# Optimization experiments

Hardware: AMD Instinct MI355X
Metric: run time of the kernel (lower is better)

The kernel has to match this reference:

```python
import math
import jax, jax.numpy as jnp
import numpy as np

B, T, D, S = 4, 8192, 1024, 32  # batch, seq, dim, num_slots; segment L = T // S


def setup_inputs() -> dict:
    key = jax.random.key(0)
    ks = jax.random.split(key, 11)
    d_inv_sqrt = D ** -0.5
    return {
        "x": jax.random.normal(ks[0], (B, T, D), jnp.float32),
        "gate_w": jax.random.normal(ks[1], (D, D), jnp.float32) * d_inv_sqrt,
        "gate_b": jnp.zeros((D,), jnp.float32),
        "read_q_w": jax.random.normal(ks[2], (D, D), jnp.float32) * 0.02,
        "read_k_w": jax.random.normal(ks[3], (D, D), jnp.float32) * 0.02,
        "read_v_w": jax.random.normal(ks[4], (D, D), jnp.float32) * 0.02,
        "output_w": jax.random.normal(ks[5], (D, D), jnp.float32) * d_inv_sqrt,
        "memory_slots": jax.random.normal(ks[6], (S, D), jnp.float32) * 0.02,
        "write_q_w": jax.random.normal(ks[7], (D, D), jnp.float32) * 0.02,
        "write_k_w": jax.random.normal(ks[8], (D, D), jnp.float32) * 0.02,
        "write_v_w": jax.random.normal(ks[9], (D, D), jnp.float32) * 0.02,
    }


def reference(x, gate_w, gate_b, read_q_w, read_k_w, read_v_w, output_w,
              memory_slots, write_q_w, write_k_w, write_v_w):
    b, t, d = x.shape
    s = memory_slots.shape[0]
    L = t // s  # segment length
    scale = 1.0 / math.sqrt(d)

    h = x @ gate_w.T + gate_b  # [B,T,D] gate pre-activation

    # --- write: per-slot attention over that slot's segment (block-diagonal) ---
    q = memory_slots @ write_q_w.T                      # [S,D]
    xs = x.reshape(b, s, L, d)                          # [B,S,L,D]
    k = xs @ write_k_w.T                                # [B,S,L,D]
    v = xs @ write_v_w.T                                # [B,S,L,D]
    wqk = jnp.einsum('sd,bsld->bsl', q, k) * scale      # [B,S,L]
    wattn = jax.nn.softmax(wqk, axis=-1)
    memory = jnp.einsum('bsl,bsld->bsd', wattn, v)      # [B,S,D]

    # --- read: masked cross-attention from tokens to memory slots ---
    rq = x @ read_q_w.T                                 # [B,T,D]
    rk = memory @ read_k_w.T                            # [B,S,D]
    rv = memory @ read_v_w.T                            # [B,S,D]
    rqk = jnp.einsum('btd,bsd->bts', rq, rk) * scale    # [B,T,S]
    seg = jnp.arange(t) // L                            # token -> segment index
    mask = seg[:, None] <= jnp.arange(s)[None, :]       # [T,S]; attend to slots >= own segment
    rqk = jnp.where(mask[None, :, :], rqk, -jnp.inf)
    rattn = jax.nn.softmax(rqk, axis=-1)
    read = jnp.einsum('bts,bsd->btd', rattn, rv)        # [B,T,D]

    y = x + jax.nn.sigmoid(h) * read
    out = y @ output_w.T
    return out, memory
```

## Files before the change

### kernel.cpp

```cpp
#include <hip/hip_runtime.h>
#include <stdint.h>

#define TB 4
#define TT 8192
#define TD 1024
#define TS 32
#define TL 256
#define BT 32768

typedef unsigned short u16;
typedef __bf16 bf16x8 __attribute__((ext_vector_type(8)));
typedef float f32x4 __attribute__((ext_vector_type(4)));

typedef uint32_t u32_g __attribute__((address_space(1)));
typedef uint32_t u32_l __attribute__((address_space(3)));

#define VMWAIT(N) asm volatile("s_waitcnt vmcnt(" #N ")" ::: "memory")
#define LGKM0()   asm volatile("s_waitcnt lgkmcnt(0)" ::: "memory")

__device__ __forceinline__ u16 f2b(float f){
  union { float f; uint32_t u; } a; a.f = f;
  uint32_t r = a.u + 0x7FFFu + ((a.u >> 16) & 1u);
  return (u16)(r >> 16);
}
__device__ __forceinline__ float b2f(u16 u){
  union { uint32_t u; float f; } a; a.u = ((uint32_t)u) << 16;
  return a.f;
}
__device__ __forceinline__ void gll16(const void* g, void* l){
  __builtin_amdgcn_global_load_lds((const u32_g*)g, (u32_l*)l, 16, 0, 0);
}

__global__ void k_convw(const float* __restrict__ s0, const float* __restrict__ s1,
                        const float* __restrict__ s2, const float* __restrict__ s3,
                        const float* __restrict__ s4, const float* __restrict__ s5,
                        const float* __restrict__ s6,
                        u16* __restrict__ d0, u16* __restrict__ d1,
                        u16* __restrict__ d2, u16* __restrict__ d3,
                        u16* __restrict__ d4, u16* __restrict__ d5,
                        u16* __restrict__ d6){
  int bid = blockIdx.x, tid = threadIdx.x;
  const float* src; u16* dst; int j;
  if (bid >= 6144){ src = s6; dst = d6; j = (bid - 6144)*256 + tid; }
  else {
    int mi = bid >> 10;
    j = (bid & 1023)*256 + tid;
    if      (mi == 0){ src = s0; dst = d0; }
    else if (mi == 1){ src = s1; dst = d1; }
    else if (mi == 2){ src = s2; dst = d2; }
    else if (mi == 3){ src = s3; dst = d3; }
    else if (mi == 4){ src = s4; dst = d4; }
    else             { src = s5; dst = d5; }
  }
  float4 v = ((const float4*)src)[j];
  ushort4 u; u.x=f2b(v.x); u.y=f2b(v.y); u.z=f2b(v.z); u.w=f2b(v.w);
  ((ushort4*)dst)[j] = u;
}

__global__ __launch_bounds__(512) void k_q32(const u16* __restrict__ msb, const u16* __restrict__ Wqb,
                                             float* __restrict__ q){
  int tid = threadIdx.x, lane = tid & 63, wv = tid >> 6;
  int r15 = lane & 15, kg = lane >> 4;
  int n0 = blockIdx.x*128 + wv*16;
  const u16* ap = msb + (size_t)r15*TD + kg*8;
  const u16* bp = Wqb + (size_t)(n0 + r15)*TD + kg*8;
  f32x4 a0 = {0,0,0,0}, a1 = {0,0,0,0};
  #pragma unroll 4
  for (int k0=0; k0<TD; k0+=32){
    bf16x8 b  = *(const bf16x8*)(bp + k0);
    bf16x8 x0 = *(const bf16x8*)(ap + k0);
    bf16x8 x1 = *(const bf16x8*)(ap + 16*TD + k0);
    a0 = __builtin_amdgcn_mfma_f32_16x16x32_bf16(x0, b, a0, 0,0,0);
    a1 = __builtin_amdgcn_mfma_f32_16x16x32_bf16(x1, b, a1, 0,0,0);
  }
  #pragma unroll
  for (int qq=0; qq<4; ++qq){
    q[(size_t)(kg*4 + qq)*TD + n0 + r15]      = a0[qq];
    q[(size_t)(16 + kg*4 + qq)*TD + n0 + r15] = a1[qq];
  }
}

__global__ __launch_bounds__(512) void k_smm128(const u16* __restrict__ A,
                                                const u16* __restrict__ W0, const u16* __restrict__ W1,
                                                float* __restrict__ oF0, u16* __restrict__ oB0,
                                                u16* __restrict__ oBT1){
  int tid = threadIdx.x, lane = tid & 63, wv = tid >> 6;
  int r15 = lane & 15, kg = lane >> 4;
  int wr = wv >> 2, wc = wv & 3;
  int n0 = blockIdx.x*128 + wc*32;
  const u16* W = blockIdx.z ? W1 : W0;
  const u16* ap = A + (size_t)(wr*64 + r15)*TD + kg*8;
  const u16* bp = W + (size_t)(n0 + r15)*TD + kg*8;
  f32x4 acc[4][2];
  #pragma unroll
  for (int i=0;i<4;i++){ f32x4 z={0,0,0,0}; acc[i][0]=z; acc[i][1]=z; }
  #pragma unroll 2
  for (int k0=0; k0<TD; k0+=32){
    bf16x8 b0 = *(const bf16x8*)(bp + k0);
    bf16x8 b1 = *(const bf16x8*)(bp + 16*TD + k0);
    bf16x8 a0 = *(const bf16x8*)(ap + k0);
    bf16x8 a1 = *(const bf16x8*)(ap + 16*TD + k0);
    bf16x8 a2 = *(const bf16x8*)(ap + 32*TD + k0);
    bf16x8 a3 = *(const bf16x8*)(ap + 48*TD + k0);
    acc[0][0] = __builtin_amdgcn_mfma_f32_16x16x32_bf16(a0, b0, acc[0][0], 0,0,0);
    acc[0][1] = __builtin_amdgcn_mfma_f32_16x16x32_bf16(a0, b1, acc[0][1], 0,0,0);
    acc[1][0] = __builtin_amdgcn_mfma_f32_16x16x32_bf16(a1, b0, acc[1][0], 0,0,0);
    acc[1][1] = __builtin_amdgcn_mfma_f32_16x16x32_bf16(a1, b1, acc[1][1], 0,0,0);
    acc[2][0] = __builtin_amdgcn_mfma_f32_16x16x32_bf16(a2, b0, acc[2][0], 0,0,0);
    acc[2][1] = __builtin_amdgcn_mfma_f32_16x16x32_bf16(a2, b1, acc[2][1], 0,0,0);
    acc[3][0] = __builtin_amdgcn_mfma_f32_16x16x32_bf16(a3, b0, acc[3][0], 0,0,0);
    acc[3][1] = __builtin_amdgcn_mfma_f32_16x16x32_bf16(a3, b1, acc[3][1], 0,0,0);
  }
  #pragma unroll
  for (int mf=0; mf<4; ++mf){
    #pragma unroll
    for (int nf=0; nf<2; ++nf){
      int n = n0 + nf*16 + r15;
      #pragma unroll
      for (int qq=0; qq<4; ++qq){
        float v = acc[mf][nf][qq];
        int m = wr*64 + mf*16 + kg*4 + qq;
        if (blockIdx.z == 0){
          if (oF0) oF0[(size_t)m*TD + n] = v;
          if (oB0) oB0[(size_t)m*TD + n] = f2b(v);
        } else {
          oBT1[((size_t)(m>>5)*TD + n)*TS + (m&31)] = f2b(v);
        }
      }
    }
  }
}

__global__ void k_prep_qk(const float* __restrict__ q, const float* __restrict__ Wk,
                          float* __restrict__ qk){
  __shared__ float sq[TD];
  __shared__ f32x4 part[4][64];
  int s = blockIdx.x;
  int tid = threadIdx.x;
  int ds = tid >> 6, e4 = tid & 63;
  int e = blockIdx.y*256 + e4*4;
  for (int i = tid; i < TD; i += 256) sq[i] = q[s*TD + i];
  __syncthreads();
  f32x4 acc = {0,0,0,0};
  int d0 = ds*256;
  #pragma unroll 4
  for (int d = d0; d < d0+256; ++d){
    float4 w = *(const float4*)(Wk + (size_t)d*TD + e);
    float sv = sq[d];
    acc[0] += sv*w.x; acc[1] += sv*w.y; acc[2] += sv*w.z; acc[3] += sv*w.w;
  }
  part[ds][e4] = acc;
  __syncthreads();
  if (ds == 0){
    f32x4 t = part[0][e4];
    f32x4 t1 = part[1][e4], t2 = part[2][e4], t3 = part[3][e4];
    const float scale = 1.0f/32.0f;
    float4 o;
    o.x = (t[0]+t1[0]+t2[0]+t3[0])*scale;
    o.y = (t[1]+t1[1]+t2[1]+t3[1])*scale;
    o.z = (t[2]+t1[2]+t2[2]+t3[2])*scale;
    o.w = (t[3]+t1[3]+t2[3]+t3[3])*scale;
    *(float4*)(qk + (size_t)s*TD + e) = o;
  }
}

__global__ void k_conv_dot(const float* __restrict__ x, const float* __restrict__ qk,
                           u16* __restrict__ xb, float* __restrict__ wqk){
  int lane = threadIdx.x & 63, wv = threadIdx.x >> 6;
  long bt0 = (long)blockIdx.x * 16;
  int sseg = (int)((bt0 & (TT-1)) >> 8);
  float qv[16];
  #pragma unroll
  for (int i=0;i<4;i++){
    float4 t = *(const float4*)(qk + (size_t)sseg*TD + i*256 + lane*4);
    qv[i*4+0]=t.x; qv[i*4+1]=t.y; qv[i*4+2]=t.z; qv[i*4+3]=t.w;
  }
  for (int tok = wv; tok < 16; tok += 4){
    long bt = bt0 + tok;
    const float* xr = x + bt*TD;
    float dot = 0.f;
    #pragma unroll
    for (int i=0;i<4;i++){
      float4 t = *(const float4*)(xr + i*256 + lane*4);
      ushort4 u; u.x=f2b(t.x); u.y=f2b(t.y); u.z=f2b(t.z); u.w=f2b(t.w);
      *(ushort4*)(xb + bt*TD + i*256 + lane*4) = u;
      dot += t.x*qv[i*4] + t.y*qv[i*4+1] + t.z*qv[i*4+2] + t.w*qv[i*4+3];
    }
    #pragma unroll
    for (int o=32;o;o>>=1) dot += __shfl_xor(dot, o);
    if (lane == 0) wqk[bt] = dot;
  }
}

__global__ void k_wattn(const float* __restrict__ wqk, const u16* __restrict__ xb,
                        u16* __restrict__ xbarb){
  __shared__ float sw[TL];
  __shared__ float red[8];
  __shared__ f32x4 part[4][64];
  int tid = threadIdx.x, lane = tid & 63, wv = tid >> 6;
  int b = blockIdx.x >> 5, s = blockIdx.x & 31;
  long base = (long)b*TT + (long)s*TL;
  float v = wqk[base + tid];
  float m = v;
  #pragma unroll
  for (int o=32;o;o>>=1) m = fmaxf(m, __shfl_xor(m, o));
  if (lane == 0) red[wv] = m;
  __syncthreads();
  m = fmaxf(fmaxf(red[0], red[1]), fmaxf(red[2], red[3]));
  float e = __expf(v - m);
  float sm = e;
  #pragma unroll
  for (int o=32;o;o>>=1) sm += __shfl_xor(sm, o);
  if (lane == 0) red[4+wv] = sm;
  __syncthreads();
  sm = red[4]+red[5]+red[6]+red[7];
  sw[tid] = e / sm;
  __syncthreads();
  int d = blockIdx.y*256 + lane*4;
  const u16* xp = xb + (base + wv*64)*TD + d;
  f32x4 acc = {0,0,0,0};
  #pragma unroll 8
  for (int i=0; i<64; ++i){
    float w = sw[wv*64 + i];
    ushort4 u = *(const ushort4*)(xp + (size_t)i*TD);
    acc[0] += w*b2f(u.x); acc[1] += w*b2f(u.y); acc[2] += w*b2f(u.z); acc[3] += w*b2f(u.w);
  }
  part[wv][lane] = acc;
  __syncthreads();
  if (wv == 0){
    f32x4 t0 = part[0][lane], t1 = part[1][lane], t2 = part[2][lane], t3 = part[3][lane];
    ushort4 o;
    o.x = f2b(t0[0]+t1[0]+t2[0]+t3[0]);
    o.y = f2b(t0[1]+t1[1]+t2[1]+t3[1]);
    o.z = f2b(t0[2]+t1[2]+t2[2]+t3[2]);
    o.w = f2b(t0[3]+t1[3]+t2[3]+t3[3]);
    *(ushort4*)(xbarb + ((size_t)b*TS + s)*TD + d) = o;
  }
}

__global__ void k_mm(const float* __restrict__ A, const float* __restrict__ W,
                     int modeT, float scale,
                     float* __restrict__ Cf, float* __restrict__ Cf2,
                     u16* __restrict__ Cb, u16* __restrict__ CbT){
  __shared__ float sA[2][TD];
  int r0 = blockIdx.x*2;
  int n = blockIdx.y*256 + threadIdx.x;
  for (int i=threadIdx.x; i<2*TD; i+=256) sA[i>>10][i&1023] = A[(size_t)r0*TD + i];
  __syncthreads();
  float acc0=0.f, acc1=0.f;
  for (int k=0;k<TD;k+=4){
    float w0 = W[(size_t)k*TD + n],     w1 = W[(size_t)(k+1)*TD + n];
    float w2 = W[(size_t)(k+2)*TD + n], w3 = W[(size_t)(k+3)*TD + n];
    float4 a0 = *(const float4*)(&sA[0][k]);
    float4 a1 = *(const float4*)(&sA[1][k]);
    acc0 += w0*a0.x + w1*a0.y + w2*a0.z + w3*a0.w;
    acc1 += w0*a1.x + w1*a1.y + w2*a1.z + w3*a1.w;
  }
  #pragma unroll
  for (int r=0;r<2;r++){
    float v = (r==0?acc0:acc1)*scale;
    int rr = r0 + r;
    size_t idx = (size_t)rr*TD + n;
    if (Cf)  Cf[idx]  = v;
    if (Cb)  Cb[idx]  = f2b(v);
  }
}

__global__ __launch_bounds__(256) void k_pattn(const u16* __restrict__ xb, const u16* __restrict__ rkb,
                                               u16* __restrict__ P){
  int tid = threadIdx.x, lane = tid & 63, wv = tid >> 6;
  long bt0 = (long)blockIdx.x * 64;
  int b = (int)(bt0 >> 13);
  int smin = (int)((bt0 & (TT-1)) >> 8);
  int r15 = lane & 15, kg = lane >> 4;

  long tw = bt0 + wv*16;
  const u16* ap  = xb  + (size_t)(tw + r15)*TD + kg*8;
  const u16* bp0 = rkb + ((size_t)(b*TS + r15))*TD + kg*8;
  const u16* bp1 = rkb + ((size_t)(b*TS + 16 + r15))*TD + kg*8;
  f32x4 p0 = {0,0,0,0}, p1 = {0,0,0,0};
  #pragma unroll 4
  for (int ks=0; ks<32; ++ks){
    bf16x8 a  = *(const bf16x8*)(ap  + ks*32);
    bf16x8 b0 = *(const bf16x8*)(bp0 + ks*32);
    bf16x8 b1 = *(const bf16x8*)(bp1 + ks*32);
    p0 = __builtin_amdgcn_mfma_f32_16x16x32_bf16(a, b0, p0, 0,0,0);
    p1 = __builtin_amdgcn_mfma_f32_16x16x32_bf16(a, b1, p1, 0,0,0);
  }
  bool msk0 = (r15 < smin), msk1 = (16 + r15 < smin);
  #pragma unroll
  for (int q=0;q<4;q++){
    float l0 = msk0 ? -1e30f : p0[q];
    float l1 = msk1 ? -1e30f : p1[q];
    float mx = fmaxf(l0, l1);
    #pragma unroll
    for (int o=1;o<16;o<<=1) mx = fmaxf(mx, __shfl_xor(mx, o));
    float e0 = msk0 ? 0.f : __expf(l0 - mx);
    float e1 = msk1 ? 0.f : __expf(l1 - mx);
    float smv = e0 + e1;
    #pragma unroll
    for (int o=1;o<16;o<<=1) smv += __shfl_xor(smv, o);
    float rs = 1.f/smv;
    long trow = tw + 4*kg + q;
    P[trow*TS + r15]      = f2b(e0*rs);
    P[trow*TS + 16 + r15] = f2b(e1*rs);
  }
}

template<bool SIG>
__global__ __launch_bounds__(512, 2) void k_gemm(const u16* __restrict__ A, const u16* __restrict__ Bw,
                                                 const float* __restrict__ bias, void* __restrict__ Cp,
                                                 const u16* __restrict__ P, const u16* __restrict__ rvT){
  __shared__ __align__(16) char sL[131072];
  int tid = threadIdx.x, lane = tid & 63, wv = tid >> 6;
  int bid = blockIdx.x;
  int wg = ((bid & 7) << 6) | (bid >> 3);
  int nt = wg & 3, mt = wg >> 2;
  int m0 = mt*256, n0 = nt*256;
  int wr = wv >> 2, wc = wv & 3;
  int r15 = lane & 15, kg = lane >> 4;

  int ard[8], brd[4];
  #pragma unroll
  for (int i=0;i<8;i++){ int row = wr*128 + i*16 + r15; ard[i] = (row*64 + kg*16) ^ ((row&7)<<4); }
  #pragma unroll
  for (int j=0;j<4;j++){ int row = wc*64  + j*16 + r15; brd[j] = (row*64 + kg*16) ^ ((row&7)<<4); }

  const u16* asrc[2]; const u16* bsrc[2]; int ldst[2];
  #pragma unroll
  for (int r=0;r<2;r++){
    int S  = (r*8 + wv)*64 + lane;
    int r1 = (S>>3)&1, r2 = (S>>4)&1;
    int r0 = ((S>>2)&1) ^ r2;
    int row = ((S>>3)<<1) | r0;
    int kh  = (S&3) ^ ((r1<<1) | r0);
    asrc[r] = A  + (size_t)(m0 + row)*TD + kh*8;
    bsrc[r] = Bw + (size_t)(n0 + row)*TD + kh*8;
    ldst[r] = (r*8 + wv)*1024;
  }

  f32x4 acc[8][4];
  #pragma unroll
  for (int i=0;i<8;i++){
    #pragma unroll
    for (int j=0;j<4;j++){ f32x4 z = {0,0,0,0}; acc[i][j] = z; }
  }

  auto stageA = [&](int t){
    char* slot = sL + (size_t)(t&3)*32768;
    int k0 = t*32;
    gll16(asrc[0] + k0, slot + ldst[0]);
    gll16(asrc[1] + k0, slot + ldst[1]);
  };
  auto stageB = [&](int t){
    char* slot = sL + (size_t)(t&3)*32768;
    int k0 = t*32;
    gll16(bsrc[0] + k0, slot + 16384 + ldst[0]);
    gll16(bsrc[1] + k0, slot + 16384 + ldst[1]);
  };

  auto tile = [&](int t, bool prefetch){
    const char* sa = sL + (size_t)(t&3)*32768;
    const char* sb = sa + 16384;
    bf16x8 bfg[4], af[4];
    #pragma unroll
    for (int j=0;j<4;j++) bfg[j] = *(const bf16x8*)(sb + brd[j]);
    #pragma unroll
    for (int i=0;i<4;i++) af[i] = *(const bf16x8*)(sa + ard[i]);
    if (prefetch) stageA(t+3);
    __builtin_amdgcn_s_barrier();
    LGKM0();
    __builtin_amdgcn_sched_barrier(0);
    __builtin_amdgcn_s_setprio(1);
    #pragma unroll
    for (int i=0;i<4;i++){
      #pragma unroll
      for (int j=0;j<4;j++)
        acc[i][j] = __builtin_amdgcn_mfma_f32_16x16x32_bf16(af[i], bfg[j], acc[i][j], 0,0,0);
    }
    __builtin_amdgcn_s_setprio(0);
    bf16x8 af2[4];
    #pragma unroll
    for (int i=0;i<4;i++) af2[i] = *(const bf16x8*)(sa + ard[4+i]);
    if (prefetch) stageB(t+3);
    __builtin_amdgcn_s_barrier();
    LGKM0();
    __builtin_amdgcn_sched_barrier(0);
    __builtin_amdgcn_s_setprio(1);
    #pragma unroll
    for (int i=0;i<4;i++){
      #pragma unroll
      for (int j=0;j<4;j++)
        acc[4+i][j] = __builtin_amdgcn_mfma_f32_16x16x32_bf16(af2[i], bfg[j], acc[4+i][j], 0,0,0);
    }
    __builtin_amdgcn_s_setprio(0);
  };

  stageA(0); stageB(0); stageA(1); stageB(1); stageA(2); stageB(2);

  for (int t=0; t<30; ++t){
    VMWAIT(8);
    __builtin_amdgcn_s_barrier();
    tile(t, t < 29);
  }
  VMWAIT(4); __builtin_amdgcn_s_barrier(); tile(30, false);
  VMWAIT(0); __builtin_amdgcn_s_barrier(); tile(31, false);

  if (SIG){
    int b = m0 >> 13;
    bf16x8 vfrag[4];
    #pragma unroll
    for (int j=0;j<4;j++){
      int n = n0 + wc*64 + j*16 + r15;
      vfrag[j] = *(const bf16x8*)(rvT + ((size_t)b*TD + n)*TS + kg*8);
    }
    #pragma unroll
    for (int i=0;i<8;i++){
      int tokbase = m0 + wr*128 + i*16;
      bf16x8 pfrag = *(const bf16x8*)(P + (size_t)(tokbase + r15)*TS + kg*8);
      f32x4 rd[4];
      #pragma unroll
      for (int j=0;j<4;j++){
        f32x4 z = {0,0,0,0};
        rd[j] = __builtin_amdgcn_mfma_f32_16x16x32_bf16(pfrag, vfrag[j], z, 0,0,0);
      }
      int mrow = tokbase + kg*4;
      #pragma unroll
      for (int j=0;j<4;j++){
        int n = n0 + wc*64 + j*16 + r15;
        float bj = bias[n];
        #pragma unroll
        for (int q=0;q<4;q++){
          float g = 1.f/(1.f + __expf(-(acc[i][j][q] + bj)));
          size_t idx = (size_t)(mrow + q)*TD + n;
          float xv = b2f(A[idx]);
          ((u16*)Cp)[idx] = f2b(xv + g*rd[j][q]);
        }
      }
    }
  } else {
    #pragma unroll
    for (int i=0;i<8;i++){
      int mrow = m0 + wr*128 + i*16 + kg*4;
      #pragma unroll
      for (int j=0;j<4;j++){
        int n = n0 + wc*64 + j*16 + r15;
        #pragma unroll
        for (int q=0;q<4;q++){
          size_t idx = (size_t)(mrow + q)*TD + n;
          ((float*)Cp)[idx] = acc[i][j][q];
        }
      }
    }
  }
}

extern "C" void kernel_launch(void* const* d_in, const int* in_sizes, int n_in,
                              void* d_out, int out_size, void* d_ws, size_t ws_size,
                              hipStream_t stream){
  const float* x   = (const float*)d_in[0];
  const float* gw  = (const float*)d_in[1];
  const float* gb  = (const float*)d_in[2];
  const float* rqw = (const float*)d_in[3];
  const float* rkw = (const float*)d_in[4];
  const float* rvw = (const float*)d_in[5];
  const float* ow  = (const float*)d_in[6];
  const float* ms  = (const float*)d_in[7];
  const float* wqw = (const float*)d_in[8];
  const float* wkw = (const float*)d_in[9];
  const float* wvw = (const float*)d_in[10];
  float* out = (float*)d_out;
  float* mem_out = out + (size_t)BT*TD;

  char* o = (char*)d_out;
  u16* xb    = (u16*)o;
  u16* Pb    = (u16*)(o + 67108864);
  u16* gwb   = (u16*)(o + 69206016);
  u16* wvwb  = (u16*)(o + 71303168);
  u16* rkwb  = (u16*)(o + 73400320);
  u16* rvwb  = (u16*)(o + 75497472);
  u16* wqwb  = (u16*)(o + 77594624);
  u16* msb   = (u16*)(o + 79691776);
  u16* xbarb = (u16*)(o + 79757312);
  u16* memb  = (u16*)(o + 80019456);
  u16* rvT   = (u16*)(o + 80281600);

  char* w = (char*)d_ws;
  u16*   gy    = (u16*)(w);
  float* wqkb  = (float*)(w + 67108864);
  float* qb    = (float*)(w + 67239936);
  float* qkb   = (float*)(w + 67371008);
  float* rkbf  = (float*)(w + 67502080);
  u16*   rkb   = (u16*)(w + 68026368);
  u16*   owb   = (u16*)(w + 68288512);

  k_convw<<<6176,256,0,stream>>>(gw, ow, wvw, rkw, rvw, wqw, ms,
                                 gwb, owb, wvwb, rkwb, rvwb, wqwb, msb);
  k_q32<<<8,512,0,stream>>>(msb, wqwb, qb);
  k_prep_qk<<<dim3(32,4),256,0,stream>>>(qb, wkw, qkb);
  k_conv_dot<<<2048,256,0,stream>>>(x, qkb, xb, wqkb);
  k_wattn<<<dim3(128,4),256,0,stream>>>(wqkb, xb, xbarb);
  k_smm128<<<dim3(8,1,1),512,0,stream>>>(xbarb, wvwb, wvwb, mem_out, memb, nullptr);
  k_smm128<<<dim3(8,1,2),512,0,stream>>>(memb, rkwb, rvwb, rkbf, nullptr, rvT);
  k_mm<<<dim3(64,4),256,0,stream>>>(rkbf, rqw, 0, 1.f/32.f, nullptr, nullptr, rkb, nullptr);
  k_pattn<<<512,256,0,stream>>>(xb, rkb, Pb);
  k_gemm<true><<<512,512,0,stream>>>(xb, gwb, gb, gy, Pb, rvT);
  k_gemm<false><<<512,512,0,stream>>>(gy, owb, nullptr, d_out, nullptr, nullptr);
}
```

Measured before the change: 458.3 us.

## Fuse weight conversion into conv_dot, convert q weights inline, stage GEMM epilogues through LDS

Five of the weight bf16 conversions now run as extra blocks of the x-conversion/dot kernel, which removes one launch. The slot-query GEMM converts fp32 inputs directly in registers, so the separate conversion of write_q_w and memory_slots is dropped. Both GEMM epilogues now stage their tiles through swizzled LDS so the residual reads and the output writes become coalesced 16-byte accesses instead of scattered scalar ones. This adds extra barriers and LDS traffic at the end of each GEMM tile.

```diff
diff --git a/kernel.cpp b/kernel.cpp
--- a/kernel.cpp
+++ b/kernel.cpp
@@ -30,46 +30,76 @@
 __device__ __forceinline__ void gll16(const void* g, void* l){
   __builtin_amdgcn_global_load_lds((const u32_g*)g, (u32_l*)l, 16, 0, 0);
 }
-
-__global__ void k_convw(const float* __restrict__ s0, const float* __restrict__ s1,
-                        const float* __restrict__ s2, const float* __restrict__ s3,
-                        const float* __restrict__ s4, const float* __restrict__ s5,
-                        const float* __restrict__ s6,
-                        u16* __restrict__ d0, u16* __restrict__ d1,
-                        u16* __restrict__ d2, u16* __restrict__ d3,
-                        u16* __restrict__ d4, u16* __restrict__ d5,
-                        u16* __restrict__ d6){
-  int bid = blockIdx.x, tid = threadIdx.x;
-  const float* src; u16* dst; int j;
-  if (bid >= 6144){ src = s6; dst = d6; j = (bid - 6144)*256 + tid; }
-  else {
-    int mi = bid >> 10;
-    j = (bid & 1023)*256 + tid;
+__device__ __forceinline__ bf16x8 cvt8(const float* p){
+  float4 a = *(const float4*)p, b = *(const float4*)(p+4);
+  union { u16 s[8]; bf16x8 v; } u;
+  u.s[0]=f2b(a.x); u.s[1]=f2b(a.y); u.s[2]=f2b(a.z); u.s[3]=f2b(a.w);
+  u.s[4]=f2b(b.x); u.s[5]=f2b(b.y); u.s[6]=f2b(b.z); u.s[7]=f2b(b.w);
+  return u.v;
+}
+
+__global__ void k_convdot(const float* __restrict__ x, const float* __restrict__ qk,
+                          u16* __restrict__ xb, float* __restrict__ wqk,
+                          const float* __restrict__ s0, const float* __restrict__ s1,
+                          const float* __restrict__ s2, const float* __restrict__ s3,
+                          const float* __restrict__ s4,
+                          u16* __restrict__ d0, u16* __restrict__ d1,
+                          u16* __restrict__ d2, u16* __restrict__ d3,
+                          u16* __restrict__ d4){
+  int tid = threadIdx.x;
+  if (blockIdx.x >= 2048){
+    int i = (blockIdx.x - 2048)*256 + tid;
+    int mi = i >> 18, j = i & 262143;
+    const float* src; u16* dst;
     if      (mi == 0){ src = s0; dst = d0; }
     else if (mi == 1){ src = s1; dst = d1; }
     else if (mi == 2){ src = s2; dst = d2; }
     else if (mi == 3){ src = s3; dst = d3; }
-    else if (mi == 4){ src = s4; dst = d4; }
-    else             { src = s5; dst = d5; }
-  }
-  float4 v = ((const float4*)src)[j];
-  ushort4 u; u.x=f2b(v.x); u.y=f2b(v.y); u.z=f2b(v.z); u.w=f2b(v.w);
-  ((ushort4*)dst)[j] = u;
-}
-
-__global__ __launch_bounds__(512) void k_q32(const u16* __restrict__ msb, const u16* __restrict__ Wqb,
-                                             float* __restrict__ q){
+    else             { src = s4; dst = d4; }
+    float4 v = ((const float4*)src)[j];
+    ushort4 u; u.x=f2b(v.x); u.y=f2b(v.y); u.z=f2b(v.z); u.w=f2b(v.w);
+    ((ushort4*)dst)[j] = u;
+    return;
+  }
+  int lane = tid & 63, wv = tid >> 6;
+  long bt0 = (long)blockIdx.x * 16;
+  int sseg = (int)((bt0 & (TT-1)) >> 8);
+  float qv[16];
+  #pragma unroll
+  for (int i=0;i<4;i++){
+    float4 t = *(const float4*)(qk + (size_t)sseg*TD + i*256 + lane*4);
+    qv[i*4+0]=t.x; qv[i*4+1]=t.y; qv[i*4+2]=t.z; qv[i*4+3]=t.w;
+  }
+  for (int tok = wv; tok < 16; tok += 4){
+    long bt = bt0 + tok;
+    const float* xr = x + bt*TD;
+    float dot = 0.f;
+    #pragma unroll
+    for (int i=0;i<4;i++){
+      float4 t = *(const float4*)(xr + i*256 + lane*4);
+      ushort4 u; u.x=f2b(t.x); u.y=f2b(t.y); u.z=f2b(t.z); u.w=f2b(t.w);
+      *(ushort4*)(xb + bt*TD + i*256 + lane*4) = u;
+      dot += t.x*qv[i*4] + t.y*qv[i*4+1] + t.z*qv[i*4+2] + t.w*qv[i*4+3];
+    }
+    #pragma unroll
+    for (int o=32;o;o>>=1) dot += __shfl_xor(dot, o);
+    if (lane == 0) wqk[bt] = dot;
+  }
+}
+
+__global__ __launch_bounds__(512) void k_q32f(const float* __restrict__ ms, const float* __restrict__ Wq,
+                                              float* __restrict__ q){
   int tid = threadIdx.x, lane = tid & 63, wv = tid >> 6;
   int r15 = lane & 15, kg = lane >> 4;
   int n0 = blockIdx.x*128 + wv*16;
-  const u16* ap = msb + (size_t)r15*TD + kg*8;
-  const u16* bp = Wqb + (size_t)(n0 + r15)*TD + kg*8;
+  const float* ap = ms + (size_t)r15*TD + kg*8;
+  const float* bp = Wq + (size_t)(n0 + r15)*TD + kg*8;
   f32x4 a0 = {0,0,0,0}, a1 = {0,0,0,0};
   #pragma unroll 4
   for (int k0=0; k0<TD; k0+=32){
-    bf16x8 b  = *(const bf16x8*)(bp + k0);
-    bf16x8 x0 = *(const bf16x8*)(ap + k0);
-    bf16x8 x1 = *(const bf16x8*)(ap + 16*TD + k0);
+    bf16x8 b  = cvt8(bp + k0);
+    bf16x8 x0 = cvt8(ap + k0);
+    bf16x8 x1 = cvt8(ap + 16*TD + k0);
     a0 = __builtin_amdgcn_mfma_f32_16x16x32_bf16(x0, b, a0, 0,0,0);
     a1 = __builtin_amdgcn_mfma_f32_16x16x32_bf16(x1, b, a1, 0,0,0);
   }
@@ -164,34 +194,6 @@
   }
 }
 
-__global__ void k_conv_dot(const float* __restrict__ x, const float* __restrict__ qk,
-                           u16* __restrict__ xb, float* __restrict__ wqk){
-  int lane = threadIdx.x & 63, wv = threadIdx.x >> 6;
-  long bt0 = (long)blockIdx.x * 16;
-  int sseg = (int)((bt0 & (TT-1)) >> 8);
-  float qv[16];
-  #pragma unroll
-  for (int i=0;i<4;i++){
-    float4 t = *(const float4*)(qk + (size_t)sseg*TD + i*256 + lane*4);
-    qv[i*4+0]=t.x; qv[i*4+1]=t.y; qv[i*4+2]=t.z; qv[i*4+3]=t.w;
-  }
-  for (int tok = wv; tok < 16; tok += 4){
-    long bt = bt0 + tok;
-    const float* xr = x + bt*TD;
-    float dot = 0.f;
-    #pragma unroll
-    for (int i=0;i<4;i++){
-      float4 t = *(const float4*)(xr + i*256 + lane*4);
-      ushort4 u; u.x=f2b(t.x); u.y=f2b(t.y); u.z=f2b(t.z); u.w=f2b(t.w);
-      *(ushort4*)(xb + bt*TD + i*256 + lane*4) = u;
-      dot += t.x*qv[i*4] + t.y*qv[i*4+1] + t.z*qv[i*4+2] + t.w*qv[i*4+3];
-    }
-    #pragma unroll
-    for (int o=32;o;o>>=1) dot += __shfl_xor(dot, o);
-    if (lane == 0) wqk[bt] = dot;
-  }
-}
-
 __global__ void k_wattn(const float* __restrict__ wqk, const u16* __restrict__ xb,
                         u16* __restrict__ xbarb){
   __shared__ float sw[TL];
@@ -406,8 +408,18 @@
   VMWAIT(4); __builtin_amdgcn_s_barrier(); tile(30, false);
   VMWAIT(0); __builtin_amdgcn_s_barrier(); tile(31, false);
 
+  __syncthreads();
+
   if (SIG){
     int b = m0 >> 13;
+    #pragma unroll
+    for (int it=0; it<16; ++it){
+      int row = it*16 + (tid>>5);
+      int c8  = (tid&31)*8;
+      bf16x8 v = *(const bf16x8*)(A + (size_t)(m0+row)*TD + n0 + c8);
+      *(bf16x8*)(sL + ((row*512 + c8*2) ^ ((row&7)<<4))) = v;
+    }
+    __syncthreads();
     bf16x8 vfrag[4];
     #pragma unroll
     for (int j=0;j<4;j++){
@@ -424,32 +436,55 @@
         f32x4 z = {0,0,0,0};
         rd[j] = __builtin_amdgcn_mfma_f32_16x16x32_bf16(pfrag, vfrag[j], z, 0,0,0);
       }
-      int mrow = tokbase + kg*4;
       #pragma unroll
       for (int j=0;j<4;j++){
-        int n = n0 + wc*64 + j*16 + r15;
-        float bj = bias[n];
+        int c = wc*64 + j*16 + r15;
+        float bj = bias[n0 + c];
         #pragma unroll
         for (int q=0;q<4;q++){
+          int r = wr*128 + i*16 + kg*4 + q;
+          int off = (r*512 + c*2) ^ ((r&7)<<4);
           float g = 1.f/(1.f + __expf(-(acc[i][j][q] + bj)));
-          size_t idx = (size_t)(mrow + q)*TD + n;
-          float xv = b2f(A[idx]);
-          ((u16*)Cp)[idx] = f2b(xv + g*rd[j][q]);
+          float xv = b2f(*(const u16*)(sL + off));
+          *(u16*)(sL + off) = f2b(xv + g*rd[j][q]);
         }
       }
     }
+    __syncthreads();
+    u16* gyp = (u16*)Cp;
+    #pragma unroll
+    for (int it=0; it<16; ++it){
+      int row = it*16 + (tid>>5);
+      int c8  = (tid&31)*8;
+      bf16x8 v = *(const bf16x8*)(sL + ((row*512 + c8*2) ^ ((row&7)<<4)));
+      *(bf16x8*)(gyp + (size_t)(m0+row)*TD + n0 + c8) = v;
+    }
   } else {
-    #pragma unroll
-    for (int i=0;i<8;i++){
-      int mrow = m0 + wr*128 + i*16 + kg*4;
+    float* op = (float*)Cp;
+    #pragma unroll
+    for (int h=0; h<2; ++h){
+      if (h) __syncthreads();
+      if (wr == h){
+        #pragma unroll
+        for (int i=0;i<8;i++){
+          #pragma unroll
+          for (int j=0;j<4;j++){
+            int c = wc*64 + j*16 + r15;
+            #pragma unroll
+            for (int q=0;q<4;q++){
+              int r = i*16 + kg*4 + q;
+              *(float*)(sL + ((r*1024 + c*4) ^ ((r&7)<<4))) = acc[i][j][q];
+            }
+          }
+        }
+      }
+      __syncthreads();
       #pragma unroll
-      for (int j=0;j<4;j++){
-        int n = n0 + wc*64 + j*16 + r15;
-        #pragma unroll
-        for (int q=0;q<4;q++){
-          size_t idx = (size_t)(mrow + q)*TD + n;
-          ((float*)Cp)[idx] = acc[i][j][q];
-        }
+      for (int it=0; it<16; ++it){
+        int r  = it*8 + (tid>>6);
+        int c4 = (tid&63)*4;
+        float4 v = *(const float4*)(sL + ((r*1024 + c4*4) ^ ((r&7)<<4)));
+        *(float4*)(op + (size_t)(m0 + h*128 + r)*TD + n0 + c4) = v;
       }
     }
   }
@@ -479,8 +514,6 @@
   u16* wvwb  = (u16*)(o + 71303168);
   u16* rkwb  = (u16*)(o + 73400320);
   u16* rvwb  = (u16*)(o + 75497472);
-  u16* wqwb  = (u16*)(o + 77594624);
-  u16* msb   = (u16*)(o + 79691776);
   u16* xbarb = (u16*)(o + 79757312);
   u16* memb  = (u16*)(o + 80019456);
   u16* rvT   = (u16*)(o + 80281600);
@@ -494,11 +527,11 @@
   u16*   rkb   = (u16*)(w + 68026368);
   u16*   owb   = (u16*)(w + 68288512);
 
-  k_convw<<<6176,256,0,stream>>>(gw, ow, wvw, rkw, rvw, wqw, ms,
-                                 gwb, owb, wvwb, rkwb, rvwb, wqwb, msb);
-  k_q32<<<8,512,0,stream>>>(msb, wqwb, qb);
+  k_q32f<<<8,512,0,stream>>>(ms, wqw, qb);
   k_prep_qk<<<dim3(32,4),256,0,stream>>>(qb, wkw, qkb);
-  k_conv_dot<<<2048,256,0,stream>>>(x, qkb, xb, wqkb);
+  k_convdot<<<7168,256,0,stream>>>(x, qkb, xb, wqkb,
+                                   gw, ow, wvw, rkw, rvw,
+                                   gwb, owb, wvwb, rkwb, rvwb);
   k_wattn<<<dim3(128,4),256,0,stream>>>(wqkb, xb, xbarb);
   k_smm128<<<dim3(8,1,1),512,0,stream>>>(xbarb, wvwb, wvwb, mem_out, memb, nullptr);
   k_smm128<<<dim3(8,1,2),512,0,stream>>>(memb, rkwb, rvwb, rkbf, nullptr, rvT);
```

Result: slower. 487.0 us (+6.2%).
